# Optimization experiments

Measured on AMD Instinct MI355X. Metric: run time of the kernel, lower is better.

The kernel has to match this reference:

```python
import jax, jax.numpy as jnp
import numpy as np

SR = 44100
DUR = 2.0
DS = 64
IN_GAIN = 10.0 ** (5.2 / 20.0)


def design_lr4_ir(freq, sr, n_taps=512):
    wc = np.tan(np.pi * freq / sr)
    wc2 = wc * wc
    root2 = np.sqrt(2.0)
    denom = 1 + root2 * wc + wc2
    b_lp = np.array([wc2 / denom, 2 * wc2 / denom, wc2 / denom])
    a_lp = np.array([1.0, 2 * (wc2 - 1) / denom, (1 - root2 * wc + wc2) / denom])
    b_hp = np.array([1 / denom, -2 / denom, 1 / denom])
    a_hp = np.array([1.0, 2 * (wc2 - 1) / denom, (1 - root2 * wc + wc2) / denom])
    b_lp4 = np.convolve(b_lp, b_lp); a_lp4 = np.convolve(a_lp, a_lp)
    b_hp4 = np.convolve(b_hp, b_hp); a_hp4 = np.convolve(a_hp, a_hp)
    def lfilter(b, a, x):
        y = np.zeros_like(x)
        for n in range(len(x)):
            acc = 0.0
            for i in range(len(b)):
                if n - i >= 0:
                    acc += b[i] * x[n - i]
            for i in range(1, len(a)):
                if n - i >= 0:
                    acc -= a[i] * y[n - i]
            y[n] = acc
        return y
    imp = np.zeros(n_taps); imp[0] = 1.0
    return lfilter(b_lp4, a_lp4, imp), lfilter(b_hp4, a_hp4, imp)


def _fir(x, w):
    # x: [B,C,T], w: flipped IR [K]; causal (left) padding, same filter per channel (grouped)
    K = w.shape[0]; C = x.shape[1]
    xp = jnp.pad(x, ((0, 0), (0, 0), (K - 1, 0)))
    kern = jnp.broadcast_to(w.reshape(1, 1, K), (C, 1, K))
    return jax.lax.conv_general_dilated(xp, kern, (1,), 'VALID',
                                        dimension_numbers=('NCH', 'OIH', 'NCH'),
                                        feature_group_count=C)


def _conv1d(x, w, b, pad, dil):
    y = jax.lax.conv_general_dilated(x, w, (1,), [(pad, pad)], rhs_dilation=(dil,),
                                     dimension_numbers=('NCH', 'OIH', 'NCH'))
    return y + b[None, :, None]


def _knee(x, thr, slope, k):
    diff = x - thr
    g_knee = slope * (diff + k / 2) ** 2 / (2 * k)
    return jnp.where(jnp.abs(diff) <= k / 2, g_knee,
                     jnp.where(diff > k / 2, slope * diff, jnp.zeros_like(x)))


def _forward(audio, params, rel_alphas, knee_db, ir_low_lp, ir_low_hp, ir_high_lp, ir_high_hp,
             w0, b0, w1, b1, w2, b2, w3, b3, w4, b4):
    batch, C, T = audio.shape
    audio_in = audio * IN_GAIN
    ott = params[:, -7:]
    amount = ott[:, 0][:, None, None]
    # 3-band LR4 crossover via 512-tap FIRs
    low = _fir(audio_in, ir_low_lp)
    m_h = _fir(audio_in, ir_low_hp)
    mid = _fir(m_h, ir_high_lp)
    high = _fir(m_h, ir_high_hp)
    bands = jnp.stack([high, mid, low], axis=1)            # [B,3,2,T]
    b_flat = bands.reshape(batch * 3, C, T)
    x_sq = jnp.mean(b_flat ** 2, axis=1, keepdims=True)    # [B3,1,T]
    Tc = T // DS
    x_rms = jnp.sqrt(x_sq[..., :Tc * DS].reshape(batch * 3, 1, Tc, DS).mean(-1) + 1e-7)
    # release-only envelope follower via cummax trick (faithful to torch code incl. repeat order)
    rel = jnp.repeat(rel_alphas, batch).reshape(-1, 1, 1)
    k = 1.0 - rel
    idx = jnp.arange(Tc, dtype=x_rms.dtype)
    kp = k ** idx
    ki = k ** (-idx)
    env_c = jax.lax.cummax(x_rms * ki, axis=2) * kp        # [B3,1,Tc]
    # linear interp back to T (align_corners=True)
    pos = jnp.arange(T, dtype=jnp.float32) * ((Tc - 1) / (T - 1))
    i0 = jnp.clip(jnp.floor(pos).astype(jnp.int32), 0, Tc - 2)
    frac = pos - i0.astype(jnp.float32)
    env = jnp.take(env_c, i0, axis=2) * (1 - frac) + jnp.take(env_c, i0 + 1, axis=2) * frac
    env_db = 20.0 * jnp.log10(env + 1e-7).reshape(batch, 3, T)
    t_a = jnp.stack([ott[:, 3], ott[:, 2], ott[:, 1]], axis=1)[..., None]
    t_b = jnp.stack([ott[:, 6], ott[:, 5], ott[:, 4]], axis=1)[..., None]
    above_slopes = jnp.array([1.0, 1.0 - 1 / 66.7, 1.0 - 1 / 66.7], jnp.float32).reshape(1, 3, 1)
    below_slope = jnp.float32(1.0 - 1.0 / 4.17)
    g_db = -_knee(env_db, t_a, above_slopes, knee_db) + _knee(-env_db, -t_b, below_slope, knee_db)
    out_gains = jnp.array([10.3, 5.7, 10.3], jnp.float32).reshape(1, 3, 1)
    total_g = 10.0 ** (jnp.clip(g_db + out_gains, -80.0, 40.0) / 20.0)
    combined = (bands * total_g[:, :, None, :]).sum(axis=1)  # [B,2,T]
    g = lambda z: jax.nn.gelu(z, approximate=False)
    r = g(_conv1d(combined, w0, b0, 1, 1))
    r = g(_conv1d(r, w1, b1, 2, 2))
    r = g(_conv1d(r, w2, b2, 4, 4))
    r = g(_conv1d(r, w3, b3, 8, 8))
    res = _conv1d(r, w4, b4, 1, 1)
    return (1.0 - amount) * audio + amount * (combined + res)


def setup_inputs() -> dict:
    B = 8
    T = int(SR * DUR)
    key = jax.random.key(0)
    ks = jax.random.split(key, 16)
    audio = jax.random.normal(ks[0], (B, 2, T), jnp.float32)
    amount = jax.random.uniform(ks[1], (B, 1), jnp.float32)
    thr = jax.random.uniform(ks[2], (B, 6), jnp.float32, minval=-40.0, maxval=0.0)
    params = jnp.concatenate([amount, thr], axis=1)
    ir_lp1, ir_hp1 = design_lr4_ir(88.3, SR)
    ir_lp2, ir_hp2 = design_lr4_ir(2500.0, SR)
    flip = lambda ir: jnp.asarray(ir[::-1].copy(), jnp.float32)
    sr_c = SR / DS
    rel_alphas = jnp.asarray(1.0 - np.exp(-1.0 / (sr_c * np.array([132.0, 282.0, 282.0]) / 1000.0)), jnp.float32)
    knee_db = jnp.float32(3.0)
    shapes = [(64, 2, 3), (64, 64, 3), (64, 64, 3), (64, 64, 3), (2, 64, 3)]
    out = {
        'audio': audio, 'params': params, 'rel_alphas': rel_alphas, 'knee_db': knee_db,
        'ir_low_lp': flip(ir_lp1), 'ir_low_hp': flip(ir_hp1),
        'ir_high_lp': flip(ir_lp2), 'ir_high_hp': flip(ir_hp2),
    }
    for i, (o, ci, kk) in enumerate(shapes):
        bound = 1.0 / np.sqrt(ci * kk)
        scale = 0.01 if i == len(shapes) - 1 else 1.0
        out[f'w{i}'] = jax.random.uniform(ks[4 + 2 * i], (o, ci, kk), jnp.float32, -bound, bound) * scale
        out[f'b{i}'] = jax.random.uniform(ks[5 + 2 * i], (o,), jnp.float32, -bound, bound) * scale
    return out


def reference(audio, params, rel_alphas, knee_db, ir_low_lp, ir_low_hp, ir_high_lp, ir_high_hp,
              w0, b0, w1, b1, w2, b2, w3, b3, w4, b4):
    return _forward(audio, params, rel_alphas, knee_db, ir_low_lp, ir_low_hp, ir_high_lp, ir_high_hp,
                    w0, b0, w1, b1, w2, b2, w3, b3, w4, b4)
```

## Files before the change

kernel.cpp:

```cpp
#include <hip/hip_runtime.h>
#include <math.h>

#define NT 88200
#define NB 8
#define TC 1378

static constexpr float IN_GAIN_F = 1.8197008586099834f;

#define OFF_A0    3072
#define OFF_A4    4096
#define OFF_ABF   5632
#define OFF_BANDS 24064
#define OFF_XRMS  4257664
#define OFF_ENV   4290736
#define OFF_WHL   4290736

typedef __attribute__((ext_vector_type(8))) short short8v;
typedef __attribute__((ext_vector_type(4))) short short4v;
typedef __attribute__((ext_vector_type(4))) float float4v;
typedef __attribute__((ext_vector_type(16))) float float16v;

__device__ __forceinline__ float gelus(float x) {
  float e = __builtin_amdgcn_exp2f(-2.4554670f * x);
  return x * __builtin_amdgcn_rcpf(1.f + e);
}
__device__ __forceinline__ short f2bf(float x) {
  unsigned int u = __float_as_uint(x);
  u += 0x7fffu + ((u >> 16) & 1u);
  return (short)(u >> 16);
}
__device__ __forceinline__ short f2bft(float x) {
  return (short)(__float_as_uint(x) >> 16);
}
__device__ __forceinline__ float bf2f(short s) {
  return __uint_as_float(((unsigned int)(unsigned short)s) << 16);
}

__global__ __launch_bounds__(256) void k_prep(
    const float* __restrict__ irLL, const float* __restrict__ irLH,
    const float* __restrict__ irHL, const float* __restrict__ irHH,
    const float* __restrict__ w0, const float* __restrict__ w1,
    const float* __restrict__ w2, const float* __restrict__ w3,
    const float* __restrict__ w4, float* __restrict__ ws)
{
  int gid = blockIdx.x * 256 + threadIdx.x;
  int task = blockIdx.y;
  if (task == 0) {
    short* whl = (short*)(ws + OFF_WHL);
    if (gid < 3072) {
      int band = gid >> 10, j = gid & 1023;
      float v = 0.f;
      if (j < 1023) {
        if (band == 2) {
          v = (j >= 511) ? irLL[j - 511] : 0.f;
        } else {
          const float* wb = (band == 0) ? irHH : irHL;
          int lo = j - 511; if (lo < 0) lo = 0;
          int hi = (j < 511) ? j : 511;
          float acc = 0.f;
          for (int i = lo; i <= hi; ++i) acc += irLH[i] * wb[j - i];
          v = acc;
        }
      }
      int entry = band * 1152 + 64 + j;
      short h = f2bf(v);
      whl[entry] = h;
      whl[entry + 4608] = f2bf(v - bf2f(h));
    } else if (gid < 4608) {
      int z = gid - 3072;
      int entry;
      if (z < 384) {
        int band = z >> 7, r = z & 127;
        entry = band * 1152 + (r < 64 ? r : 1024 + r);
      } else {
        entry = 3 * 1152 + (z - 384);
      }
      whl[entry] = 0;
      whl[entry + 4608] = 0;
    }
  } else if (task == 1) {
    if (gid >= 2048) return;
    int wq = gid >> 9;
    int lane = (gid >> 3) & 63;
    int j = gid & 7;
    int l16 = lane & 15, q = lane >> 4;
    int m = wq * 16 + l16;
    int K = q * 8 + j;
    float val = (K < 6) ? w0[(m * 2 + (K & 1)) * 3 + (K >> 1)] : 0.f;
    ((short*)(ws + OFF_A0))[gid] = f2bf(val);
  } else if (task == 2) {
    if (gid >= 3072) return;
    int s = gid >> 9;
    int lane = (gid - s * 512) >> 3;
    int j = gid & 7;
    int m = lane & 15, q = lane >> 4;
    int K = s * 32 + q * 8 + j;
    int k = K >> 6, ic = K & 63;
    float val = (m < 2) ? w4[(m * 64 + ic) * 3 + k] : 0.f;
    ((short*)(ws + OFF_A4))[gid] = f2bf(val);
  } else if (task == 6) {
    for (int r = 0; r < 3; ++r) {
      int i = gid * 3 + r;
      if (i < 24 * TC) ws[OFF_XRMS + i] = 0.f;
    }
  } else {
    int l = task - 3;
    if (gid >= 12288) return;
    const float* wl = (l == 0) ? w1 : (l == 1) ? w2 : w3;
    int ocg = gid / 6144;
    int rem = gid - ocg * 6144;
    int s = rem / 512;
    int rem2 = rem - s * 512;
    int lane = rem2 >> 3;
    int j = gid & 7;
    int m = ocg * 32 + (lane & 31);
    int k = s * 16 + ((lane >> 5) << 3) + j;
    int tap = k >> 6, ic = k & 63;
    short* ap = (short*)(ws + OFF_ABF);
    ap[l * 12288 + gid] = f2bf(wl[(m * 64 + ic) * 3 + tap]);
  }
}

#define FT 320
__global__ __launch_bounds__(256) void k_firm(const float* __restrict__ audio,
                                              float* __restrict__ ws)
{
  __shared__ short xh[4][1360];
  __shared__ __align__(16) short wt[9216];
  __shared__ float ssum[3][5];
  int bc = blockIdx.x, tile = blockIdx.y;
  int t0b = tile * FT;
  int tid = threadIdx.x;
  if (tid < 15) ssum[tid / 5][tid % 5] = 0.f;
  const uint4* wsrc = (const uint4*)((const short*)(ws + OFF_WHL));
  uint4* wdst = (uint4*)wt;
  for (int i = tid; i < 1152; i += 256) wdst[i] = wsrc[i];
  const float* x = audio + bc * NT;
  for (int i = tid; i < 1363; i += 256) {
    int g = t0b - 1022 + i;
    float v = (g >= 0 && g < NT) ? x[g] * IN_GAIN_F : 0.f;
    short h = f2bf(v);
#pragma unroll
    for (int c = 0; c < 4; ++c) {
      int idx = i - c;
      if (idx >= 0 && idx < 1360) xh[c][idx] = h;
    }
  }
  __syncthreads();

  int wave = tid >> 6, lane = tid & 63;
  int q = lane >> 4, l16 = lane & 15;
  int band = (l16 >= 10) ? 2 : (l16 >= 5 ? 1 : 0);
  if (l16 == 15) band = 3;
  int u = l16 - band * 5;
  const short* pAh = wt + band * 1152 + 64 + q * 8 - u * 16;
  const short* pAl = pAh + 4608;
  int c = l16 & 3;
  int xoff = wave * 80 + q * 8 + ((l16 >> 2) << 2);
  const short* pBh = &xh[c][xoff];
  float4v a0 = {0.f, 0.f, 0.f, 0.f};
  float4v a1 = {0.f, 0.f, 0.f, 0.f};
#pragma unroll 2
  for (int s = 0; s < 34; ++s) {
    short8v ah = *(const short8v*)(pAh + 32 * s);
    short8v al = *(const short8v*)(pAl + 32 * s);
    short4v bh0 = *(const short4v*)(pBh + 32 * s);
    short4v bh1 = *(const short4v*)(pBh + 32 * s + 4);
    short8v bh = __builtin_shufflevector(bh0, bh1, 0, 1, 2, 3, 4, 5, 6, 7);
    a0 = __builtin_amdgcn_mfma_f32_16x16x32_bf16(ah, bh, a0, 0, 0, 0);
    a1 = __builtin_amdgcn_mfma_f32_16x16x32_bf16(al, bh, a1, 0, 0, 0);
  }
  float acc[4];
#pragma unroll
  for (int r = 0; r < 4; ++r) acc[r] = a0[r] + a1[r];

  int b = bc >> 1, ch = bc & 1;
  float* bands = ws + OFF_BANDS;
#pragma unroll
  for (int r = 0; r < 4; ++r) {
    int m = q * 4 + r;
    if (m < 15) {
      int bnd = (m >= 10) ? 2 : (m >= 5 ? 1 : 0);
      int uu = m - bnd * 5;
      int t = t0b + wave * 80 + uu * 16 + l16;
      if (t < NT) bands[((b * 3 + bnd) * 2 + ch) * NT + t] = acc[r];
    }
  }

  float s2[4];
#pragma unroll
  for (int r = 0; r < 4; ++r) {
    int m = q * 4 + r;
    s2[r] = (m < 15) ? acc[r] * acc[r] : 0.f;
  }
#pragma unroll
  for (int mask = 1; mask < 16; mask <<= 1)
#pragma unroll
    for (int r = 0; r < 4; ++r)
      s2[r] += __shfl_xor(s2[r], mask, 16);
  if (l16 == 0) {
#pragma unroll
    for (int r = 0; r < 4; ++r) {
      int m = q * 4 + r;
      if (m < 15) {
        int bnd = (m >= 10) ? 2 : (m >= 5 ? 1 : 0);
        int uu = m - bnd * 5;
        int jloc = (wave * 80 + uu * 16) >> 6;
        atomicAdd(&ssum[bnd][jloc], s2[r]);
      }
    }
  }
  __syncthreads();
  if (tid < 15) {
    int bnd = tid / 5, jl = tid - bnd * 5;
    int jg = tile * 5 + jl;
    if (jg < TC) atomicAdd(&ws[OFF_XRMS + (b * 3 + bnd) * TC + jg], ssum[bnd][jl]);
  }
}

__global__ __launch_bounds__(256) void k_scan(const float* __restrict__ rel_alphas,
                                              float* __restrict__ ws)
{
  __shared__ float sA[TC], sB[TC];
  int row = blockIdx.x;
  int tid = threadIdx.x;
  float kdec = 1.f - rel_alphas[row >> 3];
  const float* xr = ws + OFF_XRMS + row * TC;
  for (int i = tid; i < TC; i += 256)
    sA[i] = sqrtf(xr[i] * (0.5f / 64.f) + 1e-7f);
  __syncthreads();
  float* in = sA; float* outp = sB;
  float kp = kdec;
  for (int off = 1; off < 2048; off <<= 1) {
    for (int i = tid; i < TC; i += 256) {
      float v = in[i];
      if (i >= off) v = fmaxf(v, in[i - off] * kp);
      outp[i] = v;
    }
    kp *= kp;
    __syncthreads();
    float* tmp = in; in = outp; outp = tmp;
  }
  float* env = ws + OFF_ENV + row * TC;
  for (int i = tid; i < TC; i += 256) env[i] = in[i];
}

#define PITCH 72
#define SPAN 128
#define TILE 96

__device__ __forceinline__ void mfma_layer32(const short* in, short* outb,
    const short* __restrict__ apk, const float* __restrict__ bias,
    const int d, int t0, int ocg, int posg, int lane)
{
  int l32 = lane & 31, hi = lane >> 5;
  float16v acc;
#pragma unroll
  for (int g = 0; g < 4; ++g) {
    float4 bv = *(const float4*)&bias[ocg * 32 + hi * 4 + g * 8];
    acc[4 * g + 0] = bv.x; acc[4 * g + 1] = bv.y;
    acc[4 * g + 2] = bv.z; acc[4 * g + 3] = bv.w;
  }
  int rbase = posg * 32 + l32;
  int rlo = rbase - d; rlo = rlo < 0 ? 0 : rlo;
  int rhi = rbase + d; rhi = rhi > SPAN - 1 ? SPAN - 1 : rhi;
  const short* pLo  = in + rlo * PITCH + hi * 8;
  const short* pMid = in + rbase * PITCH + hi * 8;
  const short* pHi  = in + rhi * PITCH + hi * 8;
  const short* ap = apk + (ocg * 12 * 64 + lane) * 8;
#pragma unroll
  for (int s = 0; s < 12; ++s) {
    short8v a = *(const short8v*)(ap + s * 512);
    int tap = s >> 2;
    const short* p = (tap == 0) ? pLo : (tap == 1) ? pMid : pHi;
    short8v bf = *(const short8v*)(p + (s & 3) * 16);
    acc = __builtin_amdgcn_mfma_f32_32x32x16_bf16(a, bf, acc, 0, 0, 0);
  }
  int t = t0 - 16 + rbase;
  bool z = (t < 0) | (t >= NT);
  short* wp = outb + rbase * PITCH + ocg * 32 + hi * 4;
#pragma unroll
  for (int g = 0; g < 4; ++g) {
    short4v r;
#pragma unroll
    for (int q = 0; q < 4; ++q)
      r[q] = f2bft(z ? 0.f : gelus(acc[4 * g + q]));
    *(short4v*)(wp + g * 8) = r;
  }
}

__global__ __launch_bounds__(512, 8) void k_convnet(
    const float* __restrict__ audio, const float* __restrict__ params,
    const float* __restrict__ kneep,
    const float* __restrict__ b0, const float* __restrict__ b1,
    const float* __restrict__ b2, const float* __restrict__ b3,
    const float* __restrict__ b4, const float* __restrict__ ws,
    float* __restrict__ out)
{
  __shared__ float cmb[2][SPAN];
  __shared__ __align__(16) char ubuf[SPAN * 8 * 2];
  __shared__ __align__(16) short actA[SPAN * PITCH];
  __shared__ __align__(16) short actB[SPAN * PITCH];
  float* gbuf = (float*)ubuf;
  short (*bfL0)[8] = (short(*)[8])ubuf;
  int tile = blockIdx.x, b = blockIdx.y;
  int t0 = tile * TILE;
  int tid = threadIdx.x;
  int wave = tid >> 6, lane = tid & 63;

  if (tid < 3 * SPAN) {
    int band = tid / SPAN, pos = tid - band * SPAN;
    int t = t0 - 16 + pos;
    float g = 0.f;
    if (t >= 0 && t < NT) {
      const float* env = ws + OFF_ENV;
      float knee = kneep[0];
      float halfk = 0.5f * knee;
      float inv2k = 1.f / (2.f * knee);
      const float scale = (float)(1377.0 / 88199.0);
      float pos_f = (float)t * scale;
      int i0 = (int)floorf(pos_f);
      i0 = i0 < 0 ? 0 : (i0 > TC - 2 ? TC - 2 : i0);
      float frac = pos_f - (float)i0;
      const int tacol[3] = {3, 2, 1};
      const int tbcol[3] = {6, 5, 4};
      const float asl[3] = {1.f, (float)(1.0 - 1.0 / 66.7), (float)(1.0 - 1.0 / 66.7)};
      const float bsl = (float)(1.0 - 1.0 / 4.17);
      const float og[3] = {10.3f, 5.7f, 10.3f};
      int row = b * 3 + band;
      float e = env[row * TC + i0] * (1.f - frac) + env[row * TC + i0 + 1] * frac;
      float edb = 6.0205999132796239f * __builtin_amdgcn_logf(e + 1e-7f);
      float ta = params[b * 7 + tacol[band]];
      float tb = params[b * 7 + tbcol[band]];
      float d1 = edb - ta;
      float gk1 = asl[band] * (d1 + halfk) * (d1 + halfk) * inv2k;
      float ka = (fabsf(d1) <= halfk) ? gk1 : (d1 > halfk ? asl[band] * d1 : 0.f);
      float d2 = tb - edb;
      float gk2 = bsl * (d2 + halfk) * (d2 + halfk) * inv2k;
      float kb = (fabsf(d2) <= halfk) ? gk2 : (d2 > halfk ? bsl * d2 : 0.f);
      float gdb = -ka + kb + og[band];
      gdb = fminf(fmaxf(gdb, -80.f), 40.f);
      g = __builtin_amdgcn_exp2f(gdb * 0.16609640474436812f);
    }
    gbuf[band * SPAN + pos] = g;
  }
  __syncthreads();

  if (tid < SPAN) {
    int t = t0 - 16 + tid;
    float c0 = 0.f, c1 = 0.f;
    if (t >= 0 && t < NT) {
      const float* bands = ws + OFF_BANDS;
#pragma unroll
      for (int band = 0; band < 3; ++band) {
        int row = b * 3 + band;
        float g = gbuf[band * SPAN + tid];
        c0 += bands[(row * 2 + 0) * NT + t] * g;
        c1 += bands[(row * 2 + 1) * NT + t] * g;
      }
    }
    cmb[0][tid] = c0;
    cmb[1][tid] = c1;
  }
  __syncthreads();

  for (int i = tid; i < SPAN * 8; i += 512) {
    int r = i >> 3, j = i & 7;
    short v = 0;
    if (j < 6) {
      int k = j >> 1, ic = j & 1;
      int src = r - 1 + k;
      if (src >= 0 && src < SPAN) v = f2bf(cmb[ic][src]);
    }
    bfL0[r][j] = v;
  }
  __syncthreads();

  int quad = lane >> 4, l16 = lane & 15;

  {
    int wq = wave & 3, half = wave >> 2;
    const short* ap0 = (const short*)(ws + OFF_A0);
    short8v a0 = *(const short8v*)&ap0[(wq * 64 + lane) * 8];
    float4 bv = *(const float4*)&b0[wq * 16 + quad * 4];
    float4v acc[4];
#pragma unroll
    for (int n = 0; n < 4; ++n) { acc[n][0] = bv.x; acc[n][1] = bv.y; acc[n][2] = bv.z; acc[n][3] = bv.w; }
    short8v zf = {0, 0, 0, 0, 0, 0, 0, 0};
#pragma unroll
    for (int n = 0; n < 4; ++n) {
      int row = (half * 4 + n) * 16 + l16;
      short8v bf = (quad == 0) ? *(const short8v*)&bfL0[row][0] : zf;
      acc[n] = __builtin_amdgcn_mfma_f32_16x16x32_bf16(a0, bf, acc[n], 0, 0, 0);
    }
    int ocb = wq * 16 + quad * 4;
#pragma unroll
    for (int n = 0; n < 4; ++n) {
      int p = (half * 4 + n) * 16 + l16;
      int t = t0 - 16 + p;
      bool z = (t < 0) | (t >= NT);
      short4v r;
#pragma unroll
      for (int rg = 0; rg < 4; ++rg)
        r[rg] = f2bft(z ? 0.f : gelus(acc[n][rg]));
      *(short4v*)&actA[p * PITCH + ocb] = r;
    }
  }
  __syncthreads();

  int ocg = wave & 1, posg = wave >> 1;
  const short* apk = (const short*)(ws + OFF_ABF);
  mfma_layer32(actA, actB, apk,          b1, 2, t0, ocg, posg, lane);
  __syncthreads();
  mfma_layer32(actB, actA, apk + 12288,  b2, 4, t0, ocg, posg, lane);
  __syncthreads();
  mfma_layer32(actA, actB, apk + 24576,  b3, 8, t0, ocg, posg, lane);
  __syncthreads();

  if (wave < 6) {
    const short* ap4 = (const short*)(ws + OFF_A4);
    float4v acc = {0.f, 0.f, 0.f, 0.f};
    if (quad == 0) { acc[0] = b4[0]; acc[1] = b4[1]; }
#pragma unroll
    for (int s = 0; s < 6; ++s) {
      short8v a4 = *(const short8v*)&ap4[(s * 64 + lane) * 8];
      int kt = s >> 1;
      int ic0 = (s & 1) * 32 + quad * 8;
      int row = 16 + wave * 16 + l16 + kt - 1;
      short8v bf = *(const short8v*)&actB[row * PITCH + ic0];
      acc = __builtin_amdgcn_mfma_f32_16x16x32_bf16(a4, bf, acc, 0, 0, 0);
    }
    if (quad == 0) {
      int t = t0 + wave * 16 + l16;
      if (t < NT) {
        float amt = params[b * 7];
#pragma unroll
        for (int r = 0; r < 2; ++r) {
          float aud = audio[(b * 2 + r) * NT + t];
          out[(b * 2 + r) * NT + t] =
              (1.f - amt) * aud + amt * (cmb[r][16 + wave * 16 + l16] + acc[r]);
        }
      }
    }
  }
}

extern "C" void kernel_launch(void* const* d_in, const int* in_sizes, int n_in,
                              void* d_out, int out_size, void* d_ws, size_t ws_size,
                              hipStream_t stream)
{
  (void)in_sizes; (void)n_in; (void)out_size; (void)ws_size;
  const float* audio = (const float*)d_in[0];
  const float* params = (const float*)d_in[1];
  const float* rel   = (const float*)d_in[2];
  const float* knee  = (const float*)d_in[3];
  const float* irLL  = (const float*)d_in[4];
  const float* irLH  = (const float*)d_in[5];
  const float* irHL  = (const float*)d_in[6];
  const float* irHH  = (const float*)d_in[7];
  const float* w0 = (const float*)d_in[8];  const float* b0 = (const float*)d_in[9];
  const float* w1 = (const float*)d_in[10]; const float* b1 = (const float*)d_in[11];
  const float* w2 = (const float*)d_in[12]; const float* b2 = (const float*)d_in[13];
  const float* w3 = (const float*)d_in[14]; const float* b3 = (const float*)d_in[15];
  const float* w4 = (const float*)d_in[16]; const float* b4 = (const float*)d_in[17];
  float* out = (float*)d_out;
  float* ws  = (float*)d_ws;

  hipLaunchKernelGGL(k_prep, dim3(48, 7), dim3(256), 0, stream,
                     irLL, irLH, irHL, irHH, w0, w1, w2, w3, w4, ws);
  hipLaunchKernelGGL(k_firm, dim3(16, 276), dim3(256), 0, stream, audio, ws);
  hipLaunchKernelGGL(k_scan, dim3(24), dim3(256), 0, stream, rel, ws);
  hipLaunchKernelGGL(k_convnet, dim3(919, 8), dim3(512), 0, stream,
                     audio, params, knee, b0, b1, b2, b3, b4, ws, out);
}
```

Measured before the change: 304.0 us.

## Process both stereo channels per FIR block to reuse weight tiles

The FIR MFMA kernel now handles both channels of a batch item in one block, loading each weight fragment once and applying it to two input tiles. The grid halves and the per-block weight staging shrinks because the unused fourth band slot is dropped, with lane 15 remapped onto an existing band row. The per-sample energy sums now combine both channels, which matches a channel-summed RMS. This raises the work per block and register pressure while cutting redundant weight loads and block count.

```diff
diff --git a/kernel.cpp b/kernel.cpp
--- a/kernel.cpp
+++ b/kernel.cpp
@@ -125,25 +125,31 @@
 __global__ __launch_bounds__(256) void k_firm(const float* __restrict__ audio,
                                               float* __restrict__ ws)
 {
-  __shared__ short xh[4][1360];
-  __shared__ __align__(16) short wt[9216];
+  __shared__ short xh[2][4][1344];
+  __shared__ __align__(16) short wt[6912];
   __shared__ float ssum[3][5];
-  int bc = blockIdx.x, tile = blockIdx.y;
+  int b = blockIdx.x, tile = blockIdx.y;
   int t0b = tile * FT;
   int tid = threadIdx.x;
   if (tid < 15) ssum[tid / 5][tid % 5] = 0.f;
-  const uint4* wsrc = (const uint4*)((const short*)(ws + OFF_WHL));
-  uint4* wdst = (uint4*)wt;
-  for (int i = tid; i < 1152; i += 256) wdst[i] = wsrc[i];
-  const float* x = audio + bc * NT;
-  for (int i = tid; i < 1363; i += 256) {
+  const short* whl = (const short*)(ws + OFF_WHL);
+  {
+    const uint4* srcH = (const uint4*)whl;
+    const uint4* srcL = (const uint4*)(whl + 4608);
+    uint4* dst = (uint4*)wt;
+    for (int i = tid; i < 432; i += 256) { dst[i] = srcH[i]; dst[432 + i] = srcL[i]; }
+  }
+  for (int i = tid; i < 1343; i += 256) {
     int g = t0b - 1022 + i;
-    float v = (g >= 0 && g < NT) ? x[g] * IN_GAIN_F : 0.f;
-    short h = f2bf(v);
-#pragma unroll
-    for (int c = 0; c < 4; ++c) {
-      int idx = i - c;
-      if (idx >= 0 && idx < 1360) xh[c][idx] = h;
+#pragma unroll
+    for (int ch = 0; ch < 2; ++ch) {
+      float v = (g >= 0 && g < NT) ? audio[(b * 2 + ch) * NT + g] * IN_GAIN_F : 0.f;
+      short h = f2bf(v);
+#pragma unroll
+      for (int c = 0; c < 4; ++c) {
+        int idx = i - c;
+        if (idx >= 0 && idx < 1344) xh[ch][c][idx] = h;
+      }
     }
   }
   __syncthreads();
@@ -151,30 +157,35 @@
   int wave = tid >> 6, lane = tid & 63;
   int q = lane >> 4, l16 = lane & 15;
   int band = (l16 >= 10) ? 2 : (l16 >= 5 ? 1 : 0);
-  if (l16 == 15) band = 3;
   int u = l16 - band * 5;
+  if (l16 == 15) { band = 2; u = 4; }
   const short* pAh = wt + band * 1152 + 64 + q * 8 - u * 16;
-  const short* pAl = pAh + 4608;
+  const short* pAl = pAh + 3456;
   int c = l16 & 3;
   int xoff = wave * 80 + q * 8 + ((l16 >> 2) << 2);
-  const short* pBh = &xh[c][xoff];
-  float4v a0 = {0.f, 0.f, 0.f, 0.f};
-  float4v a1 = {0.f, 0.f, 0.f, 0.f};
+  const short* pB0 = &xh[0][c][xoff];
+  const short* pB1 = &xh[1][c][xoff];
+  float4v a00 = {0.f,0.f,0.f,0.f}, a01 = {0.f,0.f,0.f,0.f};
+  float4v a10 = {0.f,0.f,0.f,0.f}, a11 = {0.f,0.f,0.f,0.f};
 #pragma unroll 2
   for (int s = 0; s < 34; ++s) {
     short8v ah = *(const short8v*)(pAh + 32 * s);
     short8v al = *(const short8v*)(pAl + 32 * s);
-    short4v bh0 = *(const short4v*)(pBh + 32 * s);
-    short4v bh1 = *(const short4v*)(pBh + 32 * s + 4);
-    short8v bh = __builtin_shufflevector(bh0, bh1, 0, 1, 2, 3, 4, 5, 6, 7);
-    a0 = __builtin_amdgcn_mfma_f32_16x16x32_bf16(ah, bh, a0, 0, 0, 0);
-    a1 = __builtin_amdgcn_mfma_f32_16x16x32_bf16(al, bh, a1, 0, 0, 0);
-  }
-  float acc[4];
-#pragma unroll
-  for (int r = 0; r < 4; ++r) acc[r] = a0[r] + a1[r];
-
-  int b = bc >> 1, ch = bc & 1;
+    short4v b00 = *(const short4v*)(pB0 + 32 * s);
+    short4v b01 = *(const short4v*)(pB0 + 32 * s + 4);
+    short4v b10 = *(const short4v*)(pB1 + 32 * s);
+    short4v b11 = *(const short4v*)(pB1 + 32 * s + 4);
+    short8v bh0 = __builtin_shufflevector(b00, b01, 0, 1, 2, 3, 4, 5, 6, 7);
+    short8v bh1 = __builtin_shufflevector(b10, b11, 0, 1, 2, 3, 4, 5, 6, 7);
+    a00 = __builtin_amdgcn_mfma_f32_16x16x32_bf16(ah, bh0, a00, 0, 0, 0);
+    a01 = __builtin_amdgcn_mfma_f32_16x16x32_bf16(al, bh0, a01, 0, 0, 0);
+    a10 = __builtin_amdgcn_mfma_f32_16x16x32_bf16(ah, bh1, a10, 0, 0, 0);
+    a11 = __builtin_amdgcn_mfma_f32_16x16x32_bf16(al, bh1, a11, 0, 0, 0);
+  }
+  float acc0[4], acc1[4];
+#pragma unroll
+  for (int r = 0; r < 4; ++r) { acc0[r] = a00[r] + a01[r]; acc1[r] = a10[r] + a11[r]; }
+
   float* bands = ws + OFF_BANDS;
 #pragma unroll
   for (int r = 0; r < 4; ++r) {
@@ -183,7 +194,10 @@
       int bnd = (m >= 10) ? 2 : (m >= 5 ? 1 : 0);
       int uu = m - bnd * 5;
       int t = t0b + wave * 80 + uu * 16 + l16;
-      if (t < NT) bands[((b * 3 + bnd) * 2 + ch) * NT + t] = acc[r];
+      if (t < NT) {
+        bands[((b * 3 + bnd) * 2 + 0) * NT + t] = acc0[r];
+        bands[((b * 3 + bnd) * 2 + 1) * NT + t] = acc1[r];
+      }
     }
   }
 
@@ -191,7 +205,7 @@
 #pragma unroll
   for (int r = 0; r < 4; ++r) {
     int m = q * 4 + r;
-    s2[r] = (m < 15) ? acc[r] * acc[r] : 0.f;
+    s2[r] = (m < 15) ? acc0[r] * acc0[r] + acc1[r] * acc1[r] : 0.f;
   }
 #pragma unroll
   for (int mask = 1; mask < 16; mask <<= 1)
@@ -468,7 +482,7 @@
 
   hipLaunchKernelGGL(k_prep, dim3(48, 7), dim3(256), 0, stream,
                      irLL, irLH, irHL, irHH, w0, w1, w2, w3, w4, ws);
-  hipLaunchKernelGGL(k_firm, dim3(16, 276), dim3(256), 0, stream, audio, ws);
+  hipLaunchKernelGGL(k_firm, dim3(8, 276), dim3(256), 0, stream, audio, ws);
   hipLaunchKernelGGL(k_scan, dim3(24), dim3(256), 0, stream, rel, ws);
   hipLaunchKernelGGL(k_convnet, dim3(919, 8), dim3(512), 0, stream,
                      audio, params, knee, b0, b1, b2, b3, b4, ws, out);
```

After: 317.4 us. +4.4%, slower.
